# Optimization experiments

Measured on AMD Instinct MI355X. Metric: run time of the kernel, lower is better.

The kernel has to match this reference:

```python
import jax, jax.numpy as jnp
import numpy as np


def setup_inputs() -> dict:
    key = jax.random.key(0)
    ks = jax.random.split(key, 5)
    B, C, H, W = 8, 256, 64, 64
    Cq = C // 8
    x = jax.random.normal(ks[0], (B, C, H, W), dtype=jnp.float32)
    # kaiming-uniform-ish scale for 1x1 convs (fan_in = C)
    s = float(np.sqrt(1.0 / C))
    Wq = jax.random.normal(ks[1], (Cq, C), dtype=jnp.float32) * s
    Wk = jax.random.normal(ks[2], (Cq, C), dtype=jnp.float32) * s
    Wv = jax.random.normal(ks[3], (C, C), dtype=jnp.float32) * s
    bq = jnp.zeros((Cq,), dtype=jnp.float32)
    bk = jnp.zeros((Cq,), dtype=jnp.float32)
    bv = jnp.zeros((C,), dtype=jnp.float32)
    gamma = jax.random.uniform(ks[4], (1,), dtype=jnp.float32)
    return {"x": x, "Wq": Wq, "bq": bq, "Wk": Wk, "bk": bk, "Wv": Wv, "bv": bv, "gamma": gamma}


def reference(x, Wq, bq, Wk, bk, Wv, bv, gamma):
    B, C, H, W = x.shape
    flat = x.reshape(B, C, H * W)                       # [B, C, N]
    # 1x1 conv == channel matmul
    q = jnp.einsum('oc,bcn->bon', Wq, flat) + bq[None, :, None]   # [B, C/8, N]
    k = jnp.einsum('oc,bcn->bon', Wk, flat) + bk[None, :, None]   # [B, C/8, N]
    v = jnp.einsum('oc,bcn->bon', Wv, flat) + bv[None, :, None]   # [B, C,   N]
    # query permuted to [B, N, C/8]; query_key = bmm -> [B, N, N]
    qk = jnp.einsum('bcn,bcm->bnm', q, k)               # [B, N, N]
    attn = jax.nn.softmax(qk, axis=1)                   # softmax over dim=1 (non-standard)
    out = jnp.einsum('bcn,bnm->bcm', v, attn)           # [B, C, N]
    out = out.reshape(B, C, H, W)
    return gamma[0] * out + x
```

## Files before the change

kernel.cpp:

```cpp
#include <hip/hip_runtime.h>
#include <hip/hip_bf16.h>

#define B_   8
#define C_   256
#define CQ_  32
#define N_   4096
#define OC_  320

typedef __bf16 bf16;
typedef __attribute__((ext_vector_type(8))) __bf16 bf16x8;
typedef __attribute__((ext_vector_type(4))) __bf16 bf16x4;
typedef __attribute__((ext_vector_type(4))) float f32x4;

#define QT_OFF ((size_t)0)
#define KT_OFF ((size_t)B_*N_*CQ_)
#define VB_OFF ((size_t)2*B_*N_*CQ_)
#define WB_OFF (VB_OFF + (size_t)B_*C_*N_)
#define XT_OFF (WB_OFF + (size_t)OC_*C_)
#define WS_END_BF16 (XT_OFF + (size_t)B_*N_*C_)
#define BIAS_BYTE (WS_END_BF16*2)
#define WS_BYTES (BIAS_BYTE + OC_*4)

__global__ __launch_bounds__(256) void prep_w(
    const float* __restrict__ Wq, const float* __restrict__ bq,
    const float* __restrict__ Wk, const float* __restrict__ bk,
    const float* __restrict__ Wv, const float* __restrict__ bv,
    bf16* __restrict__ ws)
{
  const int idx = blockIdx.x*256 + threadIdx.x;
  const int o = idx >> 8, c = idx & 255;
  const float v = (o < 32) ? Wq[o*C_ + c]
                : (o < 64) ? Wk[(o-32)*C_ + c]
                           : Wv[(o-64)*C_ + c];
  ws[WB_OFF + idx] = (bf16)v;
  if (idx < OC_) {
    const float bb = (idx < 32) ? bq[idx] : (idx < 64) ? bk[idx-32] : bv[idx-64];
    ((float*)((char*)ws + BIAS_BYTE))[idx] = bb;
  }
}

__global__ __launch_bounds__(256) void prep_x(
    const float* __restrict__ x, bf16* __restrict__ ws)
{
  const int b  = blockIdx.z;
  const int n  = blockIdx.x*64 + (threadIdx.x & 63);
  const int c0 = blockIdx.y*32 + (threadIdx.x >> 6)*8;
  const float* xp = x + ((size_t)b*C_ + c0)*N_ + n;
  bf16x8 pk;
  #pragma unroll
  for (int j = 0; j < 8; ++j) pk[j] = (bf16)xp[(size_t)j*N_];
  *(bf16x8*)(ws + XT_OFF + ((size_t)b*N_ + n)*C_ + c0) = pk;
}

__global__ __launch_bounds__(256) void qkv_mfma(
    const bf16* __restrict__ wsc, bf16* __restrict__ ws)
{
  const int b   = blockIdx.y;
  const int n0  = blockIdx.x * 64;
  const int tid = threadIdx.x, lane = tid & 63;
  const int w   = __builtin_amdgcn_readfirstlane(tid >> 6);
  const int lm  = lane & 15, g = lane >> 4;
  const int obase = w*80;

  const bf16*  Wb   = wsc + WB_OFF;
  const bf16*  xT   = wsc + XT_OFF + (size_t)b*N_*C_;
  const float* bias = (const float*)((const char*)wsc + BIAS_BYTE);

  f32x4 acc[5][4];
  #pragma unroll
  for (int ot = 0; ot < 5; ++ot)
    #pragma unroll
    for (int nt = 0; nt < 4; ++nt)
      acc[ot][nt] = (f32x4){0.f, 0.f, 0.f, 0.f};

  for (int kk = 0; kk < 8; ++kk) {
    bf16x8 wa[5], xf[4];
    #pragma unroll
    for (int ot = 0; ot < 5; ++ot)
      wa[ot] = *(const bf16x8*)(Wb + (size_t)(obase + ot*16 + lm)*C_ + kk*32 + g*8);
    #pragma unroll
    for (int nt = 0; nt < 4; ++nt)
      xf[nt] = *(const bf16x8*)(xT + (size_t)(n0 + nt*16 + lm)*C_ + kk*32 + g*8);
    #pragma unroll
    for (int ot = 0; ot < 5; ++ot)
      #pragma unroll
      for (int nt = 0; nt < 4; ++nt)
        acc[ot][nt] = __builtin_amdgcn_mfma_f32_16x16x32_bf16(
                        wa[ot], xf[nt], acc[ot][nt], 0, 0, 0);
  }

  float bv4[5][4];
  #pragma unroll
  for (int ot = 0; ot < 5; ++ot)
    #pragma unroll
    for (int r = 0; r < 4; ++r)
      bv4[ot][r] = bias[obase + ot*16 + g*4 + r];

  bf16* qT = ws + QT_OFF + (size_t)b*N_*CQ_;
  bf16* kT = ws + KT_OFF + (size_t)b*N_*CQ_;
  bf16* vb = ws + VB_OFF + (size_t)b*C_*N_;

  #pragma unroll
  for (int ot = 0; ot < 5; ++ot) {
    const int O = obase + ot*16;
    #pragma unroll
    for (int nt = 0; nt < 4; ++nt) {
      const int n = n0 + nt*16 + lm;
      if (O < 32) {
        bf16x4 pk;
        #pragma unroll
        for (int r = 0; r < 4; ++r) pk[r] = (bf16)(acc[ot][nt][r] + bv4[ot][r]);
        *(bf16x4*)(qT + (size_t)n*CQ_ + O + g*4) = pk;
      } else if (O < 64) {
        bf16x4 pk;
        #pragma unroll
        for (int r = 0; r < 4; ++r) pk[r] = (bf16)(acc[ot][nt][r] + bv4[ot][r]);
        *(bf16x4*)(kT + (size_t)n*CQ_ + (O - 32) + g*4) = pk;
      } else {
        #pragma unroll
        for (int r = 0; r < 4; ++r)
          vb[(size_t)(O - 64 + g*4 + r)*N_ + n] = (bf16)(acc[ot][nt][r] + bv4[ot][r]);
      }
    }
  }
}

__global__ __launch_bounds__(256) void attn_kernel(
    const bf16* __restrict__ ws, const float* __restrict__ x,
    const float* __restrict__ gamma, float* __restrict__ out)
{
  const int bid  = blockIdx.x;
  const int b    = bid & 7;
  const int m0   = (bid >> 3) << 6;
  const int tid  = threadIdx.x;
  const int lane = tid & 63;
  const int w    = __builtin_amdgcn_readfirstlane(tid >> 6);
  const int lm   = lane & 15;
  const int g    = lane >> 4;

  const bf16* qT = ws + QT_OFF + (size_t)b*N_*CQ_;
  const bf16* kT = ws + KT_OFF + (size_t)b*N_*CQ_;
  const bf16* vb = ws + VB_OFF + (size_t)b*C_*N_;

  __shared__ __align__(16) char Pb[2][64*128];
  __shared__ float red[4][64];
  __shared__ float dsh[64];

  bf16x8 kb[4];
  #pragma unroll
  for (int ms = 0; ms < 4; ++ms)
    kb[ms] = *(const bf16x8*)(kT + (size_t)(m0 + ms*16 + lm)*CQ_ + g*8);

  f32x4 acc[4][4];
  #pragma unroll
  for (int cs = 0; cs < 4; ++cs)
    #pragma unroll
    for (int ms = 0; ms < 4; ++ms)
      acc[cs][ms] = (f32x4){0.f, 0.f, 0.f, 0.f};
  float colsum[4] = {0.f, 0.f, 0.f, 0.f};

  const int c0  = w*64;
  const int swb = w*32 + g*8;
  const f32x4 zero4 = (f32x4){0.f, 0.f, 0.f, 0.f};

  for (int t = 0; t < 64; ++t) {
    const int n0 = t*64;

    bf16x8 vf[4][2];
    #pragma unroll
    for (int cs = 0; cs < 4; ++cs)
      #pragma unroll
      for (int kc = 0; kc < 2; ++kc)
        vf[cs][kc] = *(const bf16x8*)(vb + (size_t)(c0 + cs*16 + lm)*N_
                                         + n0 + kc*32 + g*8);

    bf16x8 qf = *(const bf16x8*)(qT + (size_t)(n0 + w*16 + lm)*CQ_ + g*8);
    f32x4 s[4];
    #pragma unroll
    for (int ms = 0; ms < 4; ++ms)
      s[ms] = __builtin_amdgcn_mfma_f32_16x16x32_bf16(qf, kb[ms], zero4, 0, 0, 0);

    char* pbuf = Pb[t & 1];
    #pragma unroll
    for (int ms = 0; ms < 4; ++ms) {
      float p0 = __expf(s[ms][0]);
      float p1 = __expf(s[ms][1]);
      float p2 = __expf(s[ms][2]);
      float p3 = __expf(s[ms][3]);
      colsum[ms] += (p0 + p1) + (p2 + p3);
      bf16x4 pk;
      pk[0] = (bf16)p0; pk[1] = (bf16)p1; pk[2] = (bf16)p2; pk[3] = (bf16)p3;
      const int m = lm + 16*ms;
      *(bf16x4*)(pbuf + m*128 + (swb ^ ((m & 7) << 4))) = pk;
    }
    __syncthreads();

    #pragma unroll
    for (int kc = 0; kc < 2; ++kc)
      #pragma unroll
      for (int ms = 0; ms < 4; ++ms) {
        const int m = lm + 16*ms;
        bf16x8 pf = *(const bf16x8*)(pbuf + m*128
                                     + ((kc*64 + g*16) ^ ((m & 7) << 4)));
        #pragma unroll
        for (int cs = 0; cs < 4; ++cs)
          acc[cs][ms] = __builtin_amdgcn_mfma_f32_16x16x32_bf16(
                          vf[cs][kc], pf, acc[cs][ms], 0, 0, 0);
      }
  }

  #pragma unroll
  for (int ms = 0; ms < 4; ++ms) {
    colsum[ms] += __shfl_xor(colsum[ms], 16, 64);
    colsum[ms] += __shfl_xor(colsum[ms], 32, 64);
  }
  if (lane < 16) {
    #pragma unroll
    for (int ms = 0; ms < 4; ++ms) red[w][lm + 16*ms] = colsum[ms];
  }
  __syncthreads();
  if (tid < 64) dsh[tid] = red[0][tid] + red[1][tid] + red[2][tid] + red[3][tid];
  __syncthreads();

  const float gam = gamma[0];
  float inv[4];
  #pragma unroll
  for (int ms = 0; ms < 4; ++ms) inv[ms] = gam / dsh[lm + 16*ms];

  #pragma unroll
  for (int cs = 0; cs < 4; ++cs)
    #pragma unroll
    for (int ms = 0; ms < 4; ++ms)
      #pragma unroll
      for (int r = 0; r < 4; ++r) {
        const int c = c0 + cs*16 + g*4 + r;
        const int m = m0 + 16*ms + lm;
        const size_t idx = ((size_t)b*C_ + c)*N_ + m;
        out[idx] = acc[cs][ms][r] * inv[ms] + x[idx];
      }
}

extern "C" void kernel_launch(void* const* d_in, const int* in_sizes, int n_in,
                              void* d_out, int out_size, void* d_ws, size_t ws_size,
                              hipStream_t stream) {
  const float* x     = (const float*)d_in[0];
  const float* Wq    = (const float*)d_in[1];
  const float* bq    = (const float*)d_in[2];
  const float* Wk    = (const float*)d_in[3];
  const float* bk    = (const float*)d_in[4];
  const float* Wv    = (const float*)d_in[5];
  const float* bv    = (const float*)d_in[6];
  const float* gamma = (const float*)d_in[7];
  float* out = (float*)d_out;
  bf16* ws   = (bf16*)d_ws;

  if (ws_size < WS_BYTES) return;

  prep_w<<<320, 256, 0, stream>>>(Wq, bq, Wk, bk, Wv, bv, ws);
  prep_x<<<dim3(64, 8, 8), 256, 0, stream>>>(x, ws);
  qkv_mfma<<<dim3(64, 8), 256, 0, stream>>>(ws, ws);
  attn_kernel<<<512, 256, 0, stream>>>(ws, x, gamma, out);
}
```

Baseline: 171.8 us.

## Use 512-thread attention blocks with 128-wide n tiles and exp2 softmax

Doubles the attention block to 8 waves, each owning 32 channels instead of 64, and processes 128 columns of n per iteration. Each wave computes scores for its own 16-row slice, so the P tile in shared memory doubles and the second half of V is loaded after the barrier. Pre-scales q by log2(e) so that softmax can use the raw hardware v_exp_f32 instruction instead of __expf. The aim is more waves in flight to hide memory latency and a cheaper exponential, at the cost of more shared memory per block and q being stored pre-scaled in bf16.

```diff
diff --git a/kernel.cpp b/kernel.cpp
--- a/kernel.cpp
+++ b/kernel.cpp
@@ -11,6 +11,8 @@
 typedef __attribute__((ext_vector_type(8))) __bf16 bf16x8;
 typedef __attribute__((ext_vector_type(4))) __bf16 bf16x4;
 typedef __attribute__((ext_vector_type(4))) float f32x4;
+
+#define LOG2E 1.4426950408889634f
 
 #define QT_OFF ((size_t)0)
 #define KT_OFF ((size_t)B_*N_*CQ_)
@@ -20,6 +22,12 @@
 #define WS_END_BF16 (XT_OFF + (size_t)B_*N_*C_)
 #define BIAS_BYTE (WS_END_BF16*2)
 #define WS_BYTES (BIAS_BYTE + OC_*4)
+
+__device__ inline float exp2_hw(float x) {
+  float r;
+  asm("v_exp_f32 %0, %1" : "=v"(r) : "v"(x));
+  return r;
+}
 
 __global__ __launch_bounds__(256) void prep_w(
     const float* __restrict__ Wq, const float* __restrict__ bq,
@@ -109,7 +117,8 @@
       if (O < 32) {
         bf16x4 pk;
         #pragma unroll
-        for (int r = 0; r < 4; ++r) pk[r] = (bf16)(acc[ot][nt][r] + bv4[ot][r]);
+        for (int r = 0; r < 4; ++r)
+          pk[r] = (bf16)((acc[ot][nt][r] + bv4[ot][r]) * LOG2E);
         *(bf16x4*)(qT + (size_t)n*CQ_ + O + g*4) = pk;
       } else if (O < 64) {
         bf16x4 pk;
@@ -125,7 +134,7 @@
   }
 }
 
-__global__ __launch_bounds__(256) void attn_kernel(
+__global__ __launch_bounds__(512, 4) void attn_kernel(
     const bf16* __restrict__ ws, const float* __restrict__ x,
     const float* __restrict__ gamma, float* __restrict__ out)
 {
@@ -142,8 +151,8 @@
   const bf16* kT = ws + KT_OFF + (size_t)b*N_*CQ_;
   const bf16* vb = ws + VB_OFF + (size_t)b*C_*N_;
 
-  __shared__ __align__(16) char Pb[2][64*128];
-  __shared__ float red[4][64];
+  __shared__ __align__(16) char Pb[2][64*256];
+  __shared__ float red[8][64];
   __shared__ float dsh[64];
 
   bf16x8 kb[4];
@@ -151,30 +160,30 @@
   for (int ms = 0; ms < 4; ++ms)
     kb[ms] = *(const bf16x8*)(kT + (size_t)(m0 + ms*16 + lm)*CQ_ + g*8);
 
-  f32x4 acc[4][4];
-  #pragma unroll
-  for (int cs = 0; cs < 4; ++cs)
+  f32x4 acc[2][4];
+  #pragma unroll
+  for (int cs = 0; cs < 2; ++cs)
     #pragma unroll
     for (int ms = 0; ms < 4; ++ms)
       acc[cs][ms] = (f32x4){0.f, 0.f, 0.f, 0.f};
   float colsum[4] = {0.f, 0.f, 0.f, 0.f};
 
-  const int c0  = w*64;
+  const int c0  = w*32;
   const int swb = w*32 + g*8;
   const f32x4 zero4 = (f32x4){0.f, 0.f, 0.f, 0.f};
 
-  for (int t = 0; t < 64; ++t) {
-    const int n0 = t*64;
-
-    bf16x8 vf[4][2];
-    #pragma unroll
-    for (int cs = 0; cs < 4; ++cs)
+  for (int t = 0; t < 32; ++t) {
+    const int n0 = t*128;
+
+    bf16x8 vfA[2][2];
+    #pragma unroll
+    for (int cs = 0; cs < 2; ++cs)
       #pragma unroll
       for (int kc = 0; kc < 2; ++kc)
-        vf[cs][kc] = *(const bf16x8*)(vb + (size_t)(c0 + cs*16 + lm)*N_
-                                         + n0 + kc*32 + g*8);
-
+        vfA[cs][kc] = *(const bf16x8*)(vb + (size_t)(c0 + cs*16 + lm)*N_
+                                          + n0 + kc*32 + g*8);
     bf16x8 qf = *(const bf16x8*)(qT + (size_t)(n0 + w*16 + lm)*CQ_ + g*8);
+
     f32x4 s[4];
     #pragma unroll
     for (int ms = 0; ms < 4; ++ms)
@@ -183,29 +192,38 @@
     char* pbuf = Pb[t & 1];
     #pragma unroll
     for (int ms = 0; ms < 4; ++ms) {
-      float p0 = __expf(s[ms][0]);
-      float p1 = __expf(s[ms][1]);
-      float p2 = __expf(s[ms][2]);
-      float p3 = __expf(s[ms][3]);
+      float p0 = exp2_hw(s[ms][0]);
+      float p1 = exp2_hw(s[ms][1]);
+      float p2 = exp2_hw(s[ms][2]);
+      float p3 = exp2_hw(s[ms][3]);
       colsum[ms] += (p0 + p1) + (p2 + p3);
       bf16x4 pk;
       pk[0] = (bf16)p0; pk[1] = (bf16)p1; pk[2] = (bf16)p2; pk[3] = (bf16)p3;
       const int m = lm + 16*ms;
-      *(bf16x4*)(pbuf + m*128 + (swb ^ ((m & 7) << 4))) = pk;
+      *(bf16x4*)(pbuf + m*256 + (swb ^ ((m & 7) << 4))) = pk;
     }
     __syncthreads();
 
-    #pragma unroll
-    for (int kc = 0; kc < 2; ++kc)
+    bf16x8 vfB[2][2];
+    #pragma unroll
+    for (int cs = 0; cs < 2; ++cs)
+      #pragma unroll
+      for (int kc = 0; kc < 2; ++kc)
+        vfB[cs][kc] = *(const bf16x8*)(vb + (size_t)(c0 + cs*16 + lm)*N_
+                                          + n0 + 64 + kc*32 + g*8);
+
+    #pragma unroll
+    for (int kc = 0; kc < 4; ++kc)
       #pragma unroll
       for (int ms = 0; ms < 4; ++ms) {
         const int m = lm + 16*ms;
-        bf16x8 pf = *(const bf16x8*)(pbuf + m*128
+        bf16x8 pf = *(const bf16x8*)(pbuf + m*256
                                      + ((kc*64 + g*16) ^ ((m & 7) << 4)));
         #pragma unroll
-        for (int cs = 0; cs < 4; ++cs)
+        for (int cs = 0; cs < 2; ++cs)
           acc[cs][ms] = __builtin_amdgcn_mfma_f32_16x16x32_bf16(
-                          vf[cs][kc], pf, acc[cs][ms], 0, 0, 0);
+                          (kc < 2) ? vfA[cs][kc] : vfB[cs][kc-2],
+                          pf, acc[cs][ms], 0, 0, 0);
       }
   }
 
@@ -219,7 +237,12 @@
     for (int ms = 0; ms < 4; ++ms) red[w][lm + 16*ms] = colsum[ms];
   }
   __syncthreads();
-  if (tid < 64) dsh[tid] = red[0][tid] + red[1][tid] + red[2][tid] + red[3][tid];
+  if (tid < 64) {
+    float sden = 0.f;
+    #pragma unroll
+    for (int r2 = 0; r2 < 8; ++r2) sden += red[r2][tid];
+    dsh[tid] = sden;
+  }
   __syncthreads();
 
   const float gam = gamma[0];
@@ -228,7 +251,7 @@
   for (int ms = 0; ms < 4; ++ms) inv[ms] = gam / dsh[lm + 16*ms];
 
   #pragma unroll
-  for (int cs = 0; cs < 4; ++cs)
+  for (int cs = 0; cs < 2; ++cs)
     #pragma unroll
     for (int ms = 0; ms < 4; ++ms)
       #pragma unroll
@@ -259,5 +282,5 @@
   prep_w<<<320, 256, 0, stream>>>(Wq, bq, Wk, bk, Wv, bv, ws);
   prep_x<<<dim3(64, 8, 8), 256, 0, stream>>>(x, ws);
   qkv_mfma<<<dim3(64, 8), 256, 0, stream>>>(ws, ws);
-  attn_kernel<<<512, 256, 0, stream>>>(ws, x, gamma, out);
-}
+  attn_kernel<<<512, 512, 0, stream>>>(ws, x, gamma, out);
+}
```

Result: slower. 176.2 us (+2.6%).
